# Kernel optimization log

Hardware: AMD Instinct MI355X
Metric: run time of the kernel (lower is better)

The kernel has to match this reference:

```python
import jax, jax.numpy as jnp
import numpy as np

TEMPERATURE = 8.0
WINDOW_SIZE = 256
NEG = -1e9

def setup_inputs() -> dict:
    key = jax.random.key(0)
    kq, kk, kv = jax.random.split(key, 3)
    B, H, S, D = 2, 16, 2048, 64
    q = jax.random.normal(kq, (B, H, S, D), dtype=jnp.float32)
    k = jax.random.normal(kk, (B, H, S, D), dtype=jnp.float32)
    v = jax.random.normal(kv, (B, H, S, D), dtype=jnp.float32)
    return {"q": q, "k": k, "v": v}

def _window_mask(len_q, len_k, window_size):
    # causal + sliding window: position i attends to j in [i-window+1, i]
    i = jnp.arange(len_q)[:, None]
    j = jnp.arange(len_k)[None, :]
    allowed = (j <= i) & (j > i - window_size)
    return allowed  # [len_q, len_k] bool

def reference(q, k, v):
    B, H, Sq, D = q.shape
    Sk = k.shape[2]
    attn = jnp.einsum('bhqd,bhkd->bhqk', q, k) / TEMPERATURE
    allowed = _window_mask(Sq, Sk, WINDOW_SIZE)  # window_size < len_k path
    attn = jnp.where(allowed[None, None], attn, NEG)
    attn = jax.nn.softmax(attn, axis=-1)  # dropout is identity in eval
    out = jnp.einsum('bhqk,bhkd->bhqd', attn, v)
    return (out, attn)
```

## Files before the change

kernel.cpp:

```cpp
#include <hip/hip_runtime.h>


#define S_LEN 2048
#define DHEAD 64
#define TQ 32
#define UEXT 288
#define KV_STRIDE 72
#define SC_STRIDE 292

typedef float     f4v __attribute__((ext_vector_type(4)));
typedef _Float16  h2v __attribute__((ext_vector_type(2)));
typedef _Float16  h4v __attribute__((ext_vector_type(4)));

__device__ __forceinline__ float dot2f(float aBits, float bBits, float c) {
#if __has_builtin(__builtin_amdgcn_fdot2)
  return __builtin_amdgcn_fdot2(__builtin_bit_cast(h2v, aBits),
                                __builtin_bit_cast(h2v, bBits), c, false);
#else
  h2v a = __builtin_bit_cast(h2v, aBits);
  h2v b = __builtin_bit_cast(h2v, bBits);
  return c + (float)a.x * (float)b.x + (float)a.y * (float)b.y;
#endif
}

__global__ __launch_bounds__(512, 4)
void cwa_kernel(const float* __restrict__ q, const float* __restrict__ k,
                const float* __restrict__ v, float* __restrict__ out,
                float* __restrict__ attn)
{
  __shared__ __align__(16) _Float16 kv[UEXT][KV_STRIDE];
  __shared__ __align__(16) _Float16 kq[TQ][DHEAD];
  __shared__ __align__(16) _Float16 sc[TQ][SC_STRIDE];
  __shared__ float rinv[TQ];

  const int t    = threadIdx.x;
  const int lane = t & 63;
  const int wv   = t >> 6;
  const int trow = lane >> 4;
  const int tcol = lane & 15;

  const int blk   = ((blockIdx.x & 7) << 8) + (blockIdx.x >> 3);
  const int bh    = blk >> 6;
  const int i0    = (blk & 63) * TQ;
  const int jbase = i0 - 256;

  const size_t base = (size_t)bh * (S_LEN * DHEAD);
  const float* qb = q + base;
  const float* kb = k + base;
  const float* vb = v + base;

  const f4v fzero = {0.f, 0.f, 0.f, 0.f};

  {
    const int r = t >> 4, d4 = t & 15;
    f4v f = *(const f4v*)(qb + (size_t)(i0 + r) * DHEAD + 4 * d4);
    h4v h = { (_Float16)f.x, (_Float16)f.y, (_Float16)f.z, (_Float16)f.w };
    *(h4v*)&kq[r][4 * d4] = h;
  }
  #pragma unroll 3
  for (int w = 0; w < 9; ++w) {
    const int idx = t + 512 * w;
    const int u = idx >> 4, d4 = idx & 15;
    const int j = jbase + u;
    f4v f = fzero;
    if (j >= 0 && j < S_LEN) f = *(const f4v*)(kb + (size_t)j * DHEAD + 4 * d4);
    h4v h = { (_Float16)f.x, (_Float16)f.y, (_Float16)f.z, (_Float16)f.w };
    *(h4v*)&kv[u][4 * d4] = h;
  }
  __syncthreads();

  {
    const int r = 4 * wv + trow;
    f4v qreg[8];
    #pragma unroll
    for (int x = 0; x < 8; ++x) qreg[x] = *(const f4v*)&kq[r][8 * x];

    float rs = 0.f;
    #pragma unroll 3
    for (int j18 = 0; j18 < 18; ++j18) {
      const int u = tcol + 16 * j18;
      float a = 0.f;
      #pragma unroll
      for (int x = 0; x < 8; ++x) {
        const f4v kr = *(const f4v*)&kv[u][8 * x];
        a = dot2f(qreg[x].x, kr.x, a);
        a = dot2f(qreg[x].y, kr.y, a);
        a = dot2f(qreg[x].z, kr.z, a);
        a = dot2f(qreg[x].w, kr.w, a);
      }
      const bool valid = (u >= r + 1) && (u <= r + 256) && (u >= 256 - i0);
      const float p = valid ? __expf(a * 0.125f) : 0.f;
      sc[r][u] = (_Float16)p;
      rs += p;
    }
    #pragma unroll
    for (int off = 8; off; off >>= 1) rs += __shfl_down(rs, off, 64);
    if (tcol == 0) rinv[r] = 1.f / rs;
  }
  __syncthreads();

  #pragma unroll 3
  for (int w = 0; w < 9; ++w) {
    const int idx = t + 512 * w;
    const int u = idx >> 4, d4 = idx & 15;
    const int j = jbase + u;
    f4v f = fzero;
    if (j >= 0 && j < S_LEN) f = *(const f4v*)(vb + (size_t)j * DHEAD + 4 * d4);
    h4v h = { (_Float16)f.x, (_Float16)f.y, (_Float16)f.z, (_Float16)f.w };
    *(h4v*)&kv[u][4 * d4] = h;
  }
  __syncthreads();

  float* abase = attn + (size_t)(bh * S_LEN + i0) * S_LEN;
  #pragma unroll 8
  for (int w = 0; w < 32; ++w) {
    const int flat = t + 512 * w;
    const int r  = flat >> 9;
    const int u4 = flat & 511;
    const int ir = i0 + r;
    const int glo = (ir - 255) >> 2;
    const int ghi = ir >> 2;
    if (u4 < glo || u4 > ghi)
      __builtin_nontemporal_store(fzero,
          (f4v*)(abase + (size_t)r * S_LEN + 4 * u4));
  }

  {
    f4v acc[4];
    #pragma unroll
    for (int i = 0; i < 4; ++i) acc[i] = fzero;
    const int u0 = 72 * trow;

    for (int s = 0; s < 18; ++s) {
      const int ub = u0 + 4 * s;
      h4v ph[4], vh[4];
      #pragma unroll
      for (int i = 0; i < 4; ++i) ph[i] = *(const h4v*)&sc[4 * wv + i][ub];
      #pragma unroll
      for (int e = 0; e < 4; ++e) vh[e] = *(const h4v*)&kv[ub + e][4 * tcol];
      #pragma unroll
      for (int e = 0; e < 4; ++e) {
        const f4v vv = { (float)vh[e].x, (float)vh[e].y,
                         (float)vh[e].z, (float)vh[e].w };
        #pragma unroll
        for (int i = 0; i < 4; ++i) {
          const float p = (float)ph[i][e];
          acc[i].x = fmaf(p, vv.x, acc[i].x);
          acc[i].y = fmaf(p, vv.y, acc[i].y);
          acc[i].z = fmaf(p, vv.z, acc[i].z);
          acc[i].w = fmaf(p, vv.w, acc[i].w);
        }
      }
    }
    #pragma unroll
    for (int i = 0; i < 4; ++i) {
      #pragma unroll
      for (int c = 0; c < 4; ++c) {
        float x = acc[i][c];
        x += __shfl_down(x, 32, 64);
        x += __shfl_down(x, 16, 64);
        acc[i][c] = x;
      }
    }
    if (trow == 0) {
      #pragma unroll
      for (int i = 0; i < 4; ++i) {
        const int r = 4 * wv + i;
        const float inv = rinv[r];
        f4v o = { acc[i].x * inv, acc[i].y * inv,
                  acc[i].z * inv, acc[i].w * inv };
        __builtin_nontemporal_store(o,
            (f4v*)(out + (size_t)(bh * S_LEN + i0 + r) * DHEAD + 4 * tcol));
      }
    }
  }

  #pragma unroll 4
  for (int w = 0; w < 32; ++w) {
    const int flat = t + 512 * w;
    const int r  = flat >> 9;
    const int u4 = flat & 511;
    const int ir = i0 + r;
    const int glo = (ir - 255) >> 2;
    const int ghi = ir >> 2;
    if (u4 >= glo && u4 <= ghi) {
      const float inv = rinv[r];
      const int j0 = 4 * u4;
      float va[4];
      #pragma unroll
      for (int c = 0; c < 4; ++c) {
        const int jc = j0 + c;
        int u = jc - jbase;
        u = u < 1 ? 1 : (u > 287 ? 287 : u);
        const bool in = (jc <= ir) && (jc > ir - 256);
        va[c] = in ? (float)sc[r][u] * inv : 0.f;
      }
      f4v val = { va[0], va[1], va[2], va[3] };
      __builtin_nontemporal_store(val, (f4v*)(abase + (size_t)r * S_LEN + j0));
    }
  }
}

extern "C" void kernel_launch(void* const* d_in, const int* in_sizes, int n_in,
                              void* d_out, int out_size, void* d_ws, size_t ws_size,
                              hipStream_t stream) {
  const float* q = (const float*)d_in[0];
  const float* k = (const float*)d_in[1];
  const float* v = (const float*)d_in[2];
  float* out  = (float*)d_out;
  float* attn = out + (size_t)2 * 16 * 2048 * 64;

  dim3 grid(2048), block(512);
  hipLaunchKernelGGL(cwa_kernel, grid, block, 0, stream, q, k, v, out, attn);
}
```

Before: 647.0 us.

## Remap attn row writes per 16-lane group and write window band directly

The zero-fill and band-write loops for the attention matrix now give each 16-lane group one row, so no per-iteration row or window bounds need recomputing. The in-window band is written in at most five strided vector iterations before the PV computation, replacing a 32-iteration masked scan that ran after it and did per-element clamped scalar LDS reads. Padding columns of the score buffer are zeroed so the out-of-window lanes of the band read zeros. This aims to cut wasted iterations and scalar LDS traffic and to issue the attn stores earlier, so they overlap with the PV compute.

```diff
diff --git a/kernel.cpp b/kernel.cpp
--- a/kernel.cpp
+++ b/kernel.cpp
@@ -93,6 +93,7 @@
       sc[r][u] = (_Float16)p;
       rs += p;
     }
+    if (tcol < 4) sc[r][288 + tcol] = (_Float16)0.f;
     #pragma unroll
     for (int off = 8; off; off >>= 1) rs += __shfl_down(rs, off, 64);
     if (tcol == 0) rinv[r] = 1.f / rs;
@@ -112,17 +113,32 @@
   __syncthreads();
 
   float* abase = attn + (size_t)(bh * S_LEN + i0) * S_LEN;
+  const int er  = t >> 4;
+  const int eir = i0 + er;
+  int glo = (eir - 255) >> 2;  if (glo < 0) glo = 0;
+  const int ghi = eir >> 2;
+  float* erow = abase + (size_t)er * S_LEN;
+
   #pragma unroll 8
   for (int w = 0; w < 32; ++w) {
-    const int flat = t + 512 * w;
-    const int r  = flat >> 9;
-    const int u4 = flat & 511;
-    const int ir = i0 + r;
-    const int glo = (ir - 255) >> 2;
-    const int ghi = ir >> 2;
+    const int u4 = tcol + 16 * w;
     if (u4 < glo || u4 > ghi)
-      __builtin_nontemporal_store(fzero,
-          (f4v*)(abase + (size_t)r * S_LEN + 4 * u4));
+      __builtin_nontemporal_store(fzero, (f4v*)(erow + 4 * u4));
+  }
+
+  {
+    const float inv = rinv[er];
+    #pragma unroll
+    for (int w = 0; w < 5; ++w) {
+      const int u4 = glo + tcol + 16 * w;
+      if (u4 <= ghi) {
+        const int u0 = 4 * u4 - jbase;
+        h4v ph = *(const h4v*)&sc[er][u0];
+        f4v val = { (float)ph.x * inv, (float)ph.y * inv,
+                    (float)ph.z * inv, (float)ph.w * inv };
+        __builtin_nontemporal_store(val, (f4v*)(erow + 4 * u4));
+      }
+    }
   }
 
   {
@@ -174,31 +190,6 @@
       }
     }
   }
-
-  #pragma unroll 4
-  for (int w = 0; w < 32; ++w) {
-    const int flat = t + 512 * w;
-    const int r  = flat >> 9;
-    const int u4 = flat & 511;
-    const int ir = i0 + r;
-    const int glo = (ir - 255) >> 2;
-    const int ghi = ir >> 2;
-    if (u4 >= glo && u4 <= ghi) {
-      const float inv = rinv[r];
-      const int j0 = 4 * u4;
-      float va[4];
-      #pragma unroll
-      for (int c = 0; c < 4; ++c) {
-        const int jc = j0 + c;
-        int u = jc - jbase;
-        u = u < 1 ? 1 : (u > 287 ? 287 : u);
-        const bool in = (jc <= ir) && (jc > ir - 256);
-        va[c] = in ? (float)sc[r][u] * inv : 0.f;
-      }
-      f4v val = { va[0], va[1], va[2], va[3] };
-      __builtin_nontemporal_store(val, (f4v*)(abase + (size_t)r * S_LEN + j0));
-    }
-  }
 }
 
 extern "C" void kernel_launch(void* const* d_in, const int* in_sizes, int n_in,
```

After: 612.7 us. 5.3% less time.
